# Performance work log

Measured on AMD Instinct MI355X. Metric: run time of the kernel, lower is better.

The kernel has to match this reference:

```python
import jax, jax.numpy as jnp
import numpy as np

N_STATE = 1280
N_HEAD = 20
HEAD_DIM = 64  # hardcoded in the original module
B = 1          # batch hardcoded to 1 by reshape in qkv_attention
N_CTX = 32
CACHE = 16384


def setup_inputs() -> dict:
    key = jax.random.key(0)
    ks = jax.random.split(key, 11)
    s = 0.02  # param init scale
    return {
        "x": jax.random.normal(ks[0], (B, N_CTX, N_STATE), jnp.float32),
        "self_k_cache": jax.random.normal(ks[1], (B, CACHE, N_STATE), jnp.float32),
        "self_v_cache": jax.random.normal(ks[2], (B, CACHE, N_STATE), jnp.float32),
        "positions": jnp.arange(N_CTX, dtype=jnp.int64) if jax.config.jax_enable_x64 else jnp.arange(N_CTX, dtype=jnp.int32),
        "mask": jnp.zeros((N_CTX, CACHE), jnp.float32),
        # learned parameters (Linear stores weight as [out, in]; y = x @ W.T + b)
        "Wq": jax.random.normal(ks[3], (N_STATE, N_STATE), jnp.float32) * s,
        "bq": jax.random.normal(ks[4], (N_STATE,), jnp.float32) * s,
        "Wk": jax.random.normal(ks[5], (N_STATE, N_STATE), jnp.float32) * s,  # key has no bias
        "Wv": jax.random.normal(ks[6], (N_STATE, N_STATE), jnp.float32) * s,
        "bv": jax.random.normal(ks[7], (N_STATE,), jnp.float32) * s,
        "Wout": jax.random.normal(ks[8], (N_STATE, N_STATE), jnp.float32) * s,
        "bout": jax.random.normal(ks[9], (N_STATE,), jnp.float32) * s,
    }


def reference(x, self_k_cache, self_v_cache, positions, mask,
              Wq, bq, Wk, Wv, bv, Wout, bout):
    scale2 = HEAD_DIM ** -0.5
    # projections
    q = x @ Wq.T + bq          # [B, n_ctx, n_state]
    k = x @ Wk.T               # [B, n_ctx, n_state] (no bias)
    v = x @ Wv.T + bv
    # scatter KV-cache update: self_k_cache[:, positions, :] = k
    kc = self_k_cache.at[:, positions, :].set(k)   # [B, CACHE, n_state]
    vc = self_v_cache.at[:, positions, :].set(v)
    # split heads
    qh = q.reshape(B, N_CTX, N_HEAD, HEAD_DIM).transpose(0, 2, 1, 3)  # [B,H,q,d]
    kh = kc.reshape(B, CACHE, N_HEAD, HEAD_DIM)                        # [B,k,H,d]
    vh = vc.reshape(B, CACHE, N_HEAD, HEAD_DIM)
    # attention: softmax(q k^T * scale2 + mask) v
    qk = jnp.einsum('bhqd,bkhd->bhqk', qh, kh) * scale2 + mask         # [B,H,q,k]
    w = jax.nn.softmax(qk, axis=-1)
    o = jnp.einsum('bhqk,bkhd->bqhd', w, vh).reshape(1, N_CTX, N_HEAD * HEAD_DIM)
    out = o @ Wout.T + bout
    return out, kc, vc
```

## Files before the change

kernel.cpp:

```cpp
#include <hip/hip_runtime.h>
#include <hip/hip_bf16.h>

#define H 20
#define Q 32
#define D 64
#define NSTATE 1280
#define CACHE_N 16384
#define NSPLIT 32
#define KCHUNK (CACHE_N / NSPLIT)
#define TK 64
#define NTILE (KCHUNK / TK)

typedef float f32x4 __attribute__((ext_vector_type(4)));

__device__ __forceinline__ void gemm_body(const float* __restrict__ x,
                                          const float* __restrict__ W,
                                          const float* __restrict__ bias,
                                          float* __restrict__ out,
                                          int c0, int ksplit) {
    __shared__ float xs[64][36];
    __shared__ float ws[64][66];
    const int t = threadIdx.x;
    const int rt = t >> 5;
    const int ct = t & 31;
    float acc[4][2] = {};

    const int kbeg = ksplit * 320;

    float4 xv[2], wv[4];
#pragma unroll
    for (int p = 0; p < 2; ++p) {
        int idx = t + p * 256;
        int row = idx >> 4, c4 = idx & 15;
        xv[p] = *(const float4*)(x + row * NSTATE + kbeg + c4 * 4);
    }
#pragma unroll
    for (int p = 0; p < 4; ++p) {
        int idx = t + p * 256;
        int c = idx >> 4, c4 = idx & 15;
        wv[p] = *(const float4*)(W + (long long)(c0 + c) * NSTATE + kbeg + c4 * 4);
    }

#pragma unroll 1
    for (int k0 = kbeg; k0 < kbeg + 320; k0 += 64) {
        __syncthreads();
#pragma unroll
        for (int p = 0; p < 2; ++p) {
            int idx = t + p * 256;
            int row = idx >> 4, c4 = idx & 15;
            xs[c4 * 4 + 0][row] = xv[p].x; xs[c4 * 4 + 1][row] = xv[p].y;
            xs[c4 * 4 + 2][row] = xv[p].z; xs[c4 * 4 + 3][row] = xv[p].w;
        }
#pragma unroll
        for (int p = 0; p < 4; ++p) {
            int idx = t + p * 256;
            int c = idx >> 4, c4 = idx & 15;
            ws[c4 * 4 + 0][c] = wv[p].x; ws[c4 * 4 + 1][c] = wv[p].y;
            ws[c4 * 4 + 2][c] = wv[p].z; ws[c4 * 4 + 3][c] = wv[p].w;
        }
        __syncthreads();
        if (k0 + 64 < kbeg + 320) {
            const int kn = k0 + 64;
#pragma unroll
            for (int p = 0; p < 2; ++p) {
                int idx = t + p * 256;
                int row = idx >> 4, c4 = idx & 15;
                xv[p] = *(const float4*)(x + row * NSTATE + kn + c4 * 4);
            }
#pragma unroll
            for (int p = 0; p < 4; ++p) {
                int idx = t + p * 256;
                int c = idx >> 4, c4 = idx & 15;
                wv[p] = *(const float4*)(W + (long long)(c0 + c) * NSTATE + kn + c4 * 4);
            }
        }
#pragma unroll 8
        for (int kk = 0; kk < 64; ++kk) {
            float4 xq = *(const float4*)&xs[kk][rt * 4];
            float2 wq = *(const float2*)&ws[kk][ct * 2];
            acc[0][0] += xq.x * wq.x; acc[0][1] += xq.x * wq.y;
            acc[1][0] += xq.y * wq.x; acc[1][1] += xq.y * wq.y;
            acc[2][0] += xq.z * wq.x; acc[2][1] += xq.z * wq.y;
            acc[3][0] += xq.w * wq.x; acc[3][1] += xq.w * wq.y;
        }
    }
#pragma unroll
    for (int r = 0; r < 4; ++r) {
        int i = rt * 4 + r;
#pragma unroll
        for (int cc = 0; cc < 2; ++cc) {
            int c = c0 + ct * 2 + cc;
            float val = acc[r][cc];
            if (ksplit == 0 && bias) val += bias[c];
            atomicAdd(&out[i * NSTATE + c], val);
        }
    }
}

__global__ __launch_bounds__(256, 2)
void gemm_qkv(const float* __restrict__ x,
              const float* __restrict__ Wq, const float* __restrict__ bq,
              const float* __restrict__ Wk,
              const float* __restrict__ Wv, const float* __restrict__ bv,
              float* __restrict__ q, float* __restrict__ k, float* __restrict__ v) {
    const int mat = blockIdx.z;
    const float* W; const float* bias; float* out;
    if (mat == 0)      { W = Wq; bias = bq;      out = q; }
    else if (mat == 1) { W = Wk; bias = nullptr; out = k; }
    else               { W = Wv; bias = bv;      out = v; }
    gemm_body(x, W, bias, out, blockIdx.x * 64, blockIdx.y);
}

__global__ __launch_bounds__(256, 2)
void gemm_one(const float* __restrict__ x, const float* __restrict__ W,
              const float* __restrict__ bias, float* __restrict__ out) {
    gemm_body(x, W, bias, out, blockIdx.x * 64, blockIdx.y);
}

__global__ void build_rowmap(const int* __restrict__ pos, int* __restrict__ rowmap) {
    int i = threadIdx.x;
    if (i < Q) rowmap[pos[i]] = i;
}

__global__ __launch_bounds__(256, 3)
void attn_fused(const float* __restrict__ qw,
                const float* __restrict__ kci, const float* __restrict__ vci,
                const float* __restrict__ knew, const float* __restrict__ vnew,
                const int* __restrict__ rowmap, const float* __restrict__ mask,
                float* __restrict__ kc, float* __restrict__ vc,
                float* __restrict__ mpart, float* __restrict__ lpart,
                __hip_bfloat16* __restrict__ opart) {
    const int h  = blockIdx.y;
    const int sp = blockIdx.x;
    const int j_base = sp * KCHUNK;

    __shared__ float qs[D][36];
    __shared__ float ks_[D][66];
    __shared__ float vs[TK][68];
    __shared__ float ps2[Q][TK];

    const int t  = threadIdx.x;
    const int qt = t >> 5;
    const int kt = t & 31;
    const int srow = t >> 4;
    const int c4   = t & 15;

#pragma unroll
    for (int p = 0; p < 2; ++p) {
        int idx = t + p * 256;
        int i = idx >> 4, cc = idx & 15;
        float4 v4 = *(const float4*)(qw + i * NSTATE + h * D + cc * 4);
        const float sc = 0.125f;
        qs[cc * 4 + 0][i] = v4.x * sc; qs[cc * 4 + 1][i] = v4.y * sc;
        qs[cc * 4 + 2][i] = v4.z * sc; qs[cc * 4 + 3][i] = v4.w * sc;
    }

    float m_r[4], l_r[4];
#pragma unroll
    for (int r = 0; r < 4; ++r) { m_r[r] = -1e30f; l_r[r] = 0.f; }
    float oacc[4][2] = {};

    float4 ka[4], va[4];
    float2 mk[4];
    int    sr[4];
    {
        const int j0 = j_base;
#pragma unroll
        for (int p = 0; p < 4; ++p) {
            int row = srow + 16 * p;
            long long j = j0 + row;
            sr[p] = rowmap[j];
            ka[p] = *(const float4*)(kci + j * NSTATE + h * D + c4 * 4);
            va[p] = *(const float4*)(vci + j * NSTATE + h * D + c4 * 4);
        }
#pragma unroll
        for (int r = 0; r < 4; ++r)
            mk[r] = *(const float2*)(mask + (long long)(qt * 4 + r) * CACHE_N + j0 + kt * 2);
    }

#pragma unroll 1
    for (int tile = 0; tile < NTILE; ++tile) {
        const int j0 = j_base + tile * TK;
        __syncthreads();

#pragma unroll
        for (int p = 0; p < 4; ++p) {
            if (sr[p] >= 0) {
                ka[p] = *(const float4*)(knew + (long long)sr[p] * NSTATE + h * D + c4 * 4);
                va[p] = *(const float4*)(vnew + (long long)sr[p] * NSTATE + h * D + c4 * 4);
            }
        }
#pragma unroll
        for (int p = 0; p < 4; ++p) {
            int row = srow + 16 * p;
            long long j = j0 + row;
            __builtin_nontemporal_store(*(const f32x4*)&ka[p], (f32x4*)(kc + j * NSTATE + h * D + c4 * 4));
            __builtin_nontemporal_store(*(const f32x4*)&va[p], (f32x4*)(vc + j * NSTATE + h * D + c4 * 4));
            ks_[c4 * 4 + 0][row] = ka[p].x; ks_[c4 * 4 + 1][row] = ka[p].y;
            ks_[c4 * 4 + 2][row] = ka[p].z; ks_[c4 * 4 + 3][row] = ka[p].w;
            *(float4*)&vs[row][c4 * 4] = va[p];
        }
        __syncthreads();

        float s[4][2];
#pragma unroll
        for (int r = 0; r < 4; ++r) { s[r][0] = mk[r].x; s[r][1] = mk[r].y; }

        if (tile + 1 < NTILE) {
            const int jn = j0 + TK;
#pragma unroll
            for (int p = 0; p < 4; ++p) {
                int row = srow + 16 * p;
                long long j = jn + row;
                sr[p] = rowmap[j];
                ka[p] = *(const float4*)(kci + j * NSTATE + h * D + c4 * 4);
                va[p] = *(const float4*)(vci + j * NSTATE + h * D + c4 * 4);
            }
#pragma unroll
            for (int r = 0; r < 4; ++r)
                mk[r] = *(const float2*)(mask + (long long)(qt * 4 + r) * CACHE_N + jn + kt * 2);
        }

#pragma unroll 8
        for (int d = 0; d < D; ++d) {
            float4 qv = *(const float4*)&qs[d][qt * 4];
            float2 kv = *(const float2*)&ks_[d][kt * 2];
            s[0][0] += qv.x * kv.x; s[0][1] += qv.x * kv.y;
            s[1][0] += qv.y * kv.x; s[1][1] += qv.y * kv.y;
            s[2][0] += qv.z * kv.x; s[2][1] += qv.z * kv.y;
            s[3][0] += qv.w * kv.x; s[3][1] += qv.w * kv.y;
        }

        float rmax[4];
#pragma unroll
        for (int r = 0; r < 4; ++r) rmax[r] = fmaxf(s[r][0], s[r][1]);
#pragma unroll
        for (int off = 16; off >= 1; off >>= 1)
#pragma unroll
            for (int r = 0; r < 4; ++r)
                rmax[r] = fmaxf(rmax[r], __shfl_xor(rmax[r], off, 64));

        float pr[4][2], rsum[4];
#pragma unroll
        for (int r = 0; r < 4; ++r) {
            float mn = fmaxf(m_r[r], rmax[r]);
            float a  = __expf(m_r[r] - mn);
            m_r[r]   = mn;
            pr[r][0] = __expf(s[r][0] - mn);
            pr[r][1] = __expf(s[r][1] - mn);
            rsum[r]  = pr[r][0] + pr[r][1];
            l_r[r]  *= a;
            oacc[r][0] *= a; oacc[r][1] *= a;
        }
#pragma unroll
        for (int off = 16; off >= 1; off >>= 1)
#pragma unroll
            for (int r = 0; r < 4; ++r)
                rsum[r] += __shfl_xor(rsum[r], off, 64);
#pragma unroll
        for (int r = 0; r < 4; ++r) l_r[r] += rsum[r];

#pragma unroll
        for (int r = 0; r < 4; ++r)
            *(float2*)&ps2[qt * 4 + r][kt * 2] = make_float2(pr[r][0], pr[r][1]);

#pragma unroll 4
        for (int jb = 0; jb < TK; jb += 4) {
            float4 pA = *(const float4*)&ps2[qt * 4 + 0][jb];
            float4 pB = *(const float4*)&ps2[qt * 4 + 1][jb];
            float4 pC = *(const float4*)&ps2[qt * 4 + 2][jb];
            float4 pD = *(const float4*)&ps2[qt * 4 + 3][jb];
            float pa0[4] = {pA.x, pA.y, pA.z, pA.w};
            float pa1[4] = {pB.x, pB.y, pB.z, pB.w};
            float pa2[4] = {pC.x, pC.y, pC.z, pC.w};
            float pa3[4] = {pD.x, pD.y, pD.z, pD.w};
#pragma unroll
            for (int jj = 0; jj < 4; ++jj) {
                float2 vv = *(const float2*)&vs[jb + jj][kt * 2];
                oacc[0][0] += pa0[jj] * vv.x; oacc[0][1] += pa0[jj] * vv.y;
                oacc[1][0] += pa1[jj] * vv.x; oacc[1][1] += pa1[jj] * vv.y;
                oacc[2][0] += pa2[jj] * vv.x; oacc[2][1] += pa2[jj] * vv.y;
                oacc[3][0] += pa3[jj] * vv.x; oacc[3][1] += pa3[jj] * vv.y;
            }
        }
    }

    const int pb = (h * NSPLIT + sp) * Q;
    if (kt == 0) {
#pragma unroll
        for (int r = 0; r < 4; ++r) {
            mpart[pb + qt * 4 + r] = m_r[r];
            lpart[pb + qt * 4 + r] = l_r[r];
        }
    }
#pragma unroll
    for (int r = 0; r < 4; ++r) {
        int i = qt * 4 + r;
        __hip_bfloat16 hx = __float2bfloat16(oacc[r][0]);
        __hip_bfloat16 hy = __float2bfloat16(oacc[r][1]);
        ushort2 u = make_ushort2(*(unsigned short*)&hx, *(unsigned short*)&hy);
        *(ushort2*)((unsigned short*)opart + (size_t)(pb + i) * D + kt * 2) = u;
    }
}

__global__ __launch_bounds__(64)
void attn_combine(const float* __restrict__ mpart, const float* __restrict__ lpart,
                  const __hip_bfloat16* __restrict__ opart, float* __restrict__ oattn) {
    const int i = blockIdx.x;
    const int h = blockIdx.y;
    const int d = threadIdx.x;
    float m[NSPLIT];
    float gm = -1e30f;
#pragma unroll
    for (int s = 0; s < NSPLIT; ++s) {
        m[s] = mpart[(h * NSPLIT + s) * Q + i];
        gm = fmaxf(gm, m[s]);
    }
    float l = 0.f, o = 0.f;
#pragma unroll
    for (int s = 0; s < NSPLIT; ++s) {
        float w = __expf(m[s] - gm);
        l += lpart[(h * NSPLIT + s) * Q + i] * w;
        o += __bfloat162float(opart[(size_t)((h * NSPLIT + s) * Q + i) * D + d]) * w;
    }
    oattn[i * NSTATE + h * D + d] = o / l;
}

extern "C" void kernel_launch(void* const* d_in, const int* in_sizes, int n_in,
                              void* d_out, int out_size, void* d_ws, size_t ws_size,
                              hipStream_t stream) {
    const float* x    = (const float*)d_in[0];
    const float* kci  = (const float*)d_in[1];
    const float* vci  = (const float*)d_in[2];
    const int*   pos  = (const int*)d_in[3];
    const float* mask = (const float*)d_in[4];
    const float* Wq   = (const float*)d_in[5];
    const float* bq   = (const float*)d_in[6];
    const float* Wk   = (const float*)d_in[7];
    const float* Wv   = (const float*)d_in[8];
    const float* bv   = (const float*)d_in[9];
    const float* Wout = (const float*)d_in[10];
    const float* bout = (const float*)d_in[11];

    float* out  = (float*)d_out;
    float* kc   = out + 40960;
    float* vc   = kc + CACHE_N * NSTATE;

    float* ws      = (float*)d_ws;
    float* kws     = ws;
    float* vws     = ws + 40960;
    float* qws     = ws + 81920;
    float* mpart   = ws + 122880;
    float* lpart   = ws + 143360;
    int*   rowmap  = (int*)(ws + 163840);
    __hip_bfloat16* opart = (__hip_bfloat16*)(ws + 180224);
    float* oattn   = qws;

    (void)hipMemsetAsync(ws, 0, 3 * 40960 * sizeof(float), stream);
    (void)hipMemsetAsync(out, 0, 40960 * sizeof(float), stream);
    (void)hipMemsetAsync(rowmap, 0xFF, CACHE_N * sizeof(int), stream);

    build_rowmap<<<1, 64, 0, stream>>>(pos, rowmap);

    gemm_qkv<<<dim3(NSTATE / 64, 4, 3), 256, 0, stream>>>(x, Wq, bq, Wk, Wv, bv, qws, kws, vws);

    attn_fused<<<dim3(NSPLIT, H), 256, 0, stream>>>(qws, kci, vci, kws, vws, rowmap, mask,
                                                    kc, vc, mpart, lpart, opart);

    attn_combine<<<dim3(Q, H), 64, 0, stream>>>(mpart, lpart, opart, oattn);

    gemm_one<<<dim3(NSTATE / 64, 4), 256, 0, stream>>>(oattn, Wout, bout, out);
}
```

Baseline: 396.6 us.

## Raise attention split count to 64 and build rowmap without memset

The attention kernel takes the split count as a runtime argument and uses 64 splits over the cache when the workspace is large enough. This doubles the grid (64x20 blocks) to fill the GPU better, at the cost of more partial results for the templated combine kernel to merge. The rowmap is now built by a parallel kernel that scans the positions, which replaces a memset plus a single-block scatter. The shared-memory staging is moved ahead of the nontemporal cache stores so the sync comes before the global writes.

New measurement: 412.8 us. 1.04x slower.

```diff
diff --git a/kernel.cpp b/kernel.cpp
--- a/kernel.cpp
+++ b/kernel.cpp
@@ -6,10 +6,7 @@
 #define D 64
 #define NSTATE 1280
 #define CACHE_N 16384
-#define NSPLIT 32
-#define KCHUNK (CACHE_N / NSPLIT)
 #define TK 64
-#define NTILE (KCHUNK / TK)
 
 typedef float f32x4 __attribute__((ext_vector_type(4)));
 
@@ -118,8 +115,12 @@
 }
 
 __global__ void build_rowmap(const int* __restrict__ pos, int* __restrict__ rowmap) {
-    int i = threadIdx.x;
-    if (i < Q) rowmap[pos[i]] = i;
+    int j = blockIdx.x * 256 + threadIdx.x;
+    int v = -1;
+#pragma unroll
+    for (int i = 0; i < Q; ++i)
+        if (pos[i] == j) v = i;
+    rowmap[j] = v;
 }
 
 __global__ __launch_bounds__(256, 3)
@@ -129,10 +130,12 @@
                 const int* __restrict__ rowmap, const float* __restrict__ mask,
                 float* __restrict__ kc, float* __restrict__ vc,
                 float* __restrict__ mpart, float* __restrict__ lpart,
-                __hip_bfloat16* __restrict__ opart) {
+                __hip_bfloat16* __restrict__ opart, int nsplit) {
     const int h  = blockIdx.y;
     const int sp = blockIdx.x;
-    const int j_base = sp * KCHUNK;
+    const int kchunk = CACHE_N / nsplit;
+    const int ntile  = kchunk / TK;
+    const int j_base = sp * kchunk;
 
     __shared__ float qs[D][36];
     __shared__ float ks_[D][66];
@@ -179,7 +182,7 @@
     }
 
 #pragma unroll 1
-    for (int tile = 0; tile < NTILE; ++tile) {
+    for (int tile = 0; tile < ntile; ++tile) {
         const int j0 = j_base + tile * TK;
         __syncthreads();
 
@@ -190,23 +193,28 @@
                 va[p] = *(const float4*)(vnew + (long long)sr[p] * NSTATE + h * D + c4 * 4);
             }
         }
+#pragma unroll
+        for (int p = 0; p < 4; ++p) {
+            int row = srow + 16 * p;
+            ks_[c4 * 4 + 0][row] = ka[p].x; ks_[c4 * 4 + 1][row] = ka[p].y;
+            ks_[c4 * 4 + 2][row] = ka[p].z; ks_[c4 * 4 + 3][row] = ka[p].w;
+            *(float4*)&vs[row][c4 * 4] = va[p];
+        }
+        __syncthreads();
+
 #pragma unroll
         for (int p = 0; p < 4; ++p) {
             int row = srow + 16 * p;
             long long j = j0 + row;
             __builtin_nontemporal_store(*(const f32x4*)&ka[p], (f32x4*)(kc + j * NSTATE + h * D + c4 * 4));
             __builtin_nontemporal_store(*(const f32x4*)&va[p], (f32x4*)(vc + j * NSTATE + h * D + c4 * 4));
-            ks_[c4 * 4 + 0][row] = ka[p].x; ks_[c4 * 4 + 1][row] = ka[p].y;
-            ks_[c4 * 4 + 2][row] = ka[p].z; ks_[c4 * 4 + 3][row] = ka[p].w;
-            *(float4*)&vs[row][c4 * 4] = va[p];
-        }
-        __syncthreads();
+        }
 
         float s[4][2];
 #pragma unroll
         for (int r = 0; r < 4; ++r) { s[r][0] = mk[r].x; s[r][1] = mk[r].y; }
 
-        if (tile + 1 < NTILE) {
+        if (tile + 1 < ntile) {
             const int jn = j0 + TK;
 #pragma unroll
             for (int p = 0; p < 4; ++p) {
@@ -285,7 +293,7 @@
         }
     }
 
-    const int pb = (h * NSPLIT + sp) * Q;
+    const int pb = (h * nsplit + sp) * Q;
     if (kt == 0) {
 #pragma unroll
         for (int r = 0; r < 4; ++r) {
@@ -303,25 +311,26 @@
     }
 }
 
+template <int NS>
 __global__ __launch_bounds__(64)
 void attn_combine(const float* __restrict__ mpart, const float* __restrict__ lpart,
                   const __hip_bfloat16* __restrict__ opart, float* __restrict__ oattn) {
     const int i = blockIdx.x;
     const int h = blockIdx.y;
     const int d = threadIdx.x;
-    float m[NSPLIT];
+    float m[NS];
     float gm = -1e30f;
 #pragma unroll
-    for (int s = 0; s < NSPLIT; ++s) {
-        m[s] = mpart[(h * NSPLIT + s) * Q + i];
+    for (int s = 0; s < NS; ++s) {
+        m[s] = mpart[(h * NS + s) * Q + i];
         gm = fmaxf(gm, m[s]);
     }
     float l = 0.f, o = 0.f;
 #pragma unroll
-    for (int s = 0; s < NSPLIT; ++s) {
+    for (int s = 0; s < NS; ++s) {
         float w = __expf(m[s] - gm);
-        l += lpart[(h * NSPLIT + s) * Q + i] * w;
-        o += __bfloat162float(opart[(size_t)((h * NSPLIT + s) * Q + i) * D + d]) * w;
+        l += lpart[(h * NS + s) * Q + i] * w;
+        o += __bfloat162float(opart[(size_t)((h * NS + s) * Q + i) * D + d]) * w;
     }
     oattn[i * NSTATE + h * D + d] = o / l;
 }
@@ -346,28 +355,33 @@
     float* kc   = out + 40960;
     float* vc   = kc + CACHE_N * NSTATE;
 
+    const size_t need64 = (size_t)221184 * 4 + (size_t)H * 64 * Q * D * 2;
+    const int ns = (ws_size >= need64) ? 64 : 32;
+
     float* ws      = (float*)d_ws;
     float* kws     = ws;
     float* vws     = ws + 40960;
     float* qws     = ws + 81920;
     float* mpart   = ws + 122880;
-    float* lpart   = ws + 143360;
-    int*   rowmap  = (int*)(ws + 163840);
-    __hip_bfloat16* opart = (__hip_bfloat16*)(ws + 180224);
+    float* lpart   = mpart + H * ns * Q;
+    int*   rowmap  = (int*)(lpart + H * ns * Q);
+    __hip_bfloat16* opart = (__hip_bfloat16*)(rowmap + CACHE_N);
     float* oattn   = qws;
 
     (void)hipMemsetAsync(ws, 0, 3 * 40960 * sizeof(float), stream);
     (void)hipMemsetAsync(out, 0, 40960 * sizeof(float), stream);
-    (void)hipMemsetAsync(rowmap, 0xFF, CACHE_N * sizeof(int), stream);
-
-    build_rowmap<<<1, 64, 0, stream>>>(pos, rowmap);
+
+    build_rowmap<<<CACHE_N / 256, 256, 0, stream>>>(pos, rowmap);
 
     gemm_qkv<<<dim3(NSTATE / 64, 4, 3), 256, 0, stream>>>(x, Wq, bq, Wk, Wv, bv, qws, kws, vws);
 
-    attn_fused<<<dim3(NSPLIT, H), 256, 0, stream>>>(qws, kci, vci, kws, vws, rowmap, mask,
-                                                    kc, vc, mpart, lpart, opart);
-
-    attn_combine<<<dim3(Q, H), 64, 0, stream>>>(mpart, lpart, opart, oattn);
+    attn_fused<<<dim3(ns, H), 256, 0, stream>>>(qws, kci, vci, kws, vws, rowmap, mask,
+                                                kc, vc, mpart, lpart, opart, ns);
+
+    if (ns == 64)
+        attn_combine<64><<<dim3(Q, H), 64, 0, stream>>>(mpart, lpart, opart, oattn);
+    else
+        attn_combine<32><<<dim3(Q, H), 64, 0, stream>>>(mpart, lpart, opart, oattn);
 
     gemm_one<<<dim3(NSTATE / 64, 4), 256, 0, stream>>>(oattn, Wout, bout, out);
 }
```
